# Kernel tuning notes

Measured on AMD Instinct MI355X. Metric: run time of the kernel, lower is better.

Reference implementation:

```python
import jax, jax.numpy as jnp
import numpy as np

B, NN, DEG = 64, 256, 8
N = B * NN
E = N * DEG
IN_N, IN_E = 128, 16
TOOL, PROC = 16, 12
TP = TOOL * PROC
H1 = 384

def _lin(key, i, o, s=0.05):
    k1, k2 = jax.random.split(key)
    return (jax.random.normal(k1, (i, o), jnp.float32) * s,
            jax.random.normal(k2, (o,), jnp.float32) * s)

def setup_inputs():
    ks = jax.random.split(jax.random.key(0), 40)
    inp = {}
    inp["ns"] = jax.random.normal(ks[0], (N, IN_N), jnp.float32)
    inp["es"] = jax.random.normal(ks[1], (E, IN_E), jnp.float32)
    inp["dm"] = jax.random.normal(ks[2], (N, NN), jnp.float32)
    inp["mask_fv"] = (jax.random.uniform(ks[3], (N, TP)) > 0.3).astype(jnp.float32)
    dst = jnp.repeat(jnp.arange(N, dtype=jnp.int32), DEG)  # fixed in-degree DEG
    src = (dst // NN) * NN + jax.random.randint(ks[4], (E,), 0, NN, dtype=jnp.int32)
    inp["src"], inp["dst"] = src, dst
    sizes = [(IN_N, H1), (H1 + 32, H1), (H1, TP)]
    for i, (cin, cout) in enumerate(sizes, 1):
        inp[f"Wm{i}"], inp[f"bm{i}"] = _lin(ks[5 + 3 * i], 2 * cin + IN_E, cin)
        inp[f"Wu{i}"], inp[f"bu{i}"] = _lin(ks[6 + 3 * i], 5 * cin, cout)
        inp[f"bng{i}"] = jnp.ones((cout,), jnp.float32)
        inp[f"bnb{i}"] = jnp.zeros((cout,), jnp.float32)
        inp[f"Wx{i}"], inp[f"bx{i}"] = _lin(ks[7 + 3 * i], cout, cout)
    inp["W1"], inp["b1"] = _lin(ks[20], NN, 64)
    inp["W2"], inp["b2"] = _lin(ks[21], 64, 32)
    inp["W3"], inp["b3"] = _lin(ks[22], NN, 64)
    inp["W4"], inp["b4"] = _lin(ks[23], 64, NN)
    return inp

def pna_conv(src, dst, h, e, Wm, bm, Wu, bu, bng, bnb, Wx, bx, relu_out):
    # DGL PNAConvTower: msg = M(cat(h_src, h_dst, e)); aggregate mean/max/sum/std per dst node;
    # U(cat(h, aggs)); BatchNorm (training stats); mixing Linear + LeakyReLU(0.01).
    cin = h.shape[1]
    msg = h[src] @ Wm[:cin] + h[dst] @ Wm[cin:2 * cin] + e @ Wm[2 * cin:] + bm  # [E, cin]
    cnt = jax.ops.segment_sum(jnp.ones((msg.shape[0],), msg.dtype), dst, N)[:, None]
    s = jax.ops.segment_sum(msg, dst, N)
    mean = s / cnt
    mx = jax.ops.segment_max(msg, dst, N)
    msq = jax.ops.segment_sum(msg * msg, dst, N) / cnt
    std = jnp.sqrt(jax.nn.relu(msq - mean * mean) + 1e-30)
    u = jnp.concatenate([h, mean, mx, s, std], axis=-1) @ Wu + bu  # [N, cout]
    u = (u - u.mean(0)) / jnp.sqrt(u.var(0) + 1e-5) * bng + bnb  # BatchNorm1d, training mode
    out = jax.nn.leaky_relu(u @ Wx + bx, 0.01)  # mixing layer
    return jax.nn.relu(out) if relu_out else out

def reference(ns, es, dm, mask_fv, Wm1, bm1, Wu1, bu1, bng1, bnb1, Wx1, bx1, Wm2, bm2, Wu2, bu2, bng2, bnb2, Wx2, bx2, Wm3, bm3, Wu3, bu3, bng3, bnb3, Wx3, bx3, W1, b1, W2, b2, W3, b3, W4, b4, src, dst):
    d2 = (dm @ W1 + b1) @ W2 + b2  # [N, 32]
    h1 = pna_conv(src, dst, ns, es, Wm1, bm1, Wu1, bu1, bng1, bnb1, Wx1, bx1, True)
    h2 = pna_conv(src, dst, jnp.concatenate([h1, d2], -1), es, Wm2, bm2, Wu2, bu2, bng2, bnb2, Wx2, bx2, True)
    h3 = pna_conv(src, dst, h2, es, Wm3, bm3, Wu3, bu3, bng3, bnb3, Wx3, bx3, False)  # [N, TP]
    nm = h3.max(-1).reshape(B, NN)
    g = jax.nn.sigmoid(jax.nn.relu(nm @ W3 + b3) @ W4 + b4)  # [B, NN]
    feat = (g.reshape(N, 1) * h3).reshape(B, -1)  # [B, NN*TP]
    feat = jnp.where(mask_fv.reshape(B, -1) == 0, -1e5, feat)
    return jax.nn.softmax(feat, -1)
```

## Files before the change

### kernel.cpp

```cpp
#include <hip/hip_runtime.h>
#include <hip/hip_bf16.h>

#define NNODE 16384

typedef short v8s __attribute__((ext_vector_type(8)));
typedef float v4f __attribute__((ext_vector_type(4)));

__device__ __forceinline__ unsigned short f2bf(float v) {
    unsigned u = __float_as_uint(v);
    unsigned r = (u + 0x7FFF + ((u >> 16) & 1)) >> 16;
    return (unsigned short)r;
}
__device__ __forceinline__ float bf2f(unsigned short s) {
    return __uint_as_float(((unsigned)s) << 16);
}

template<int EPI, int OUT, int BM>
__global__ __launch_bounds__(256, 3)
void mgemm4(const unsigned short* __restrict__ Ah, const unsigned short* __restrict__ Al,
            int ldA, int K,
            const unsigned short* __restrict__ Bh, const unsigned short* __restrict__ Bl,
            int Kpad,
            float* __restrict__ Cf, unsigned short* __restrict__ Ch, unsigned short* __restrict__ Cl,
            int ldC, int Ncol, const float* __restrict__ bias)
{
    constexpr int MF = BM / 32;
    __shared__ __align__(16) unsigned short AhS[BM * 64];
    __shared__ __align__(16) unsigned short AlS[BM * 64];
    __shared__ __align__(16) unsigned short BhS[64 * 64];
    __shared__ __align__(16) unsigned short BlS[64 * 64];
    const int bm = blockIdx.x * BM;
    const int bn = blockIdx.y * 64;
    const int tid = threadIdx.x;
    const int lane = tid & 63, wid = tid >> 6;
    const int wm = wid >> 1, wn = wid & 1;
    const int r16 = lane & 15, q = lane >> 4;
    v4f acc[MF][2];
#pragma unroll
    for (int i = 0; i < MF; i++)
#pragma unroll
        for (int j = 0; j < 2; j++) acc[i][j] = (v4f){0.f, 0.f, 0.f, 0.f};

    const int srow = tid >> 3;
    const int sc8  = tid & 7;
    const int nK = (K + 63) >> 6;
    for (int s = 0; s < nK; s++) {
        const int k0 = s << 6;
#pragma unroll
        for (int p = 0; p < BM / 32; p++) {
            int row = p * 32 + srow;
            size_t go = (size_t)(bm + row) * ldA + k0 + sc8 * 8;
            v8s hv = *(const v8s*)(const void*)(Ah + go);
            v8s lv = *(const v8s*)(const void*)(Al + go);
            int bo = row * 128 + ((sc8 * 16) ^ ((row & 7) << 4));
            *(v8s*)(void*)((char*)AhS + bo) = hv;
            *(v8s*)(void*)((char*)AlS + bo) = lv;
        }
#pragma unroll
        for (int p = 0; p < 2; p++) {
            int row = p * 32 + srow;
            size_t go = (size_t)(bn + row) * Kpad + k0 + sc8 * 8;
            v8s hv = *(const v8s*)(const void*)(Bh + go);
            v8s lv = *(const v8s*)(const void*)(Bl + go);
            int bo = row * 128 + ((sc8 * 16) ^ ((row & 7) << 4));
            *(v8s*)(void*)((char*)BhS + bo) = hv;
            *(v8s*)(void*)((char*)BlS + bo) = lv;
        }
        __syncthreads();
#pragma unroll
        for (int kc = 0; kc < 2; kc++) {
            v8s bh[2], bl[2];
#pragma unroll
            for (int nf = 0; nf < 2; nf++) {
                int bcol = wn * 32 + nf * 16 + r16;
                int bo = bcol * 128 + (((kc * 64) + q * 16) ^ ((bcol & 7) << 4));
                bh[nf] = *(const v8s*)(const void*)((const char*)BhS + bo);
                bl[nf] = *(const v8s*)(const void*)((const char*)BlS + bo);
            }
#pragma unroll
            for (int mf = 0; mf < MF; mf++) {
                int arow = wm * (BM / 2) + mf * 16 + r16;
                int ao = arow * 128 + (((kc * 64) + q * 16) ^ ((arow & 7) << 4));
                v8s ah = *(const v8s*)(const void*)((const char*)AhS + ao);
                v8s al = *(const v8s*)(const void*)((const char*)AlS + ao);
#pragma unroll
                for (int nf = 0; nf < 2; nf++) {
                    acc[mf][nf] = __builtin_amdgcn_mfma_f32_16x16x32_bf16(ah, bh[nf], acc[mf][nf], 0, 0, 0);
                    acc[mf][nf] = __builtin_amdgcn_mfma_f32_16x16x32_bf16(al, bh[nf], acc[mf][nf], 0, 0, 0);
                    acc[mf][nf] = __builtin_amdgcn_mfma_f32_16x16x32_bf16(ah, bl[nf], acc[mf][nf], 0, 0, 0);
                }
            }
        }
        __syncthreads();
    }
#pragma unroll
    for (int mf = 0; mf < MF; mf++)
#pragma unroll
        for (int nf = 0; nf < 2; nf++) {
            int col = bn + wn * 32 + nf * 16 + r16;
            if (col < Ncol) {
                float bv = bias ? bias[col] : 0.f;
#pragma unroll
                for (int r = 0; r < 4; r++) {
                    int row = bm + wm * (BM / 2) + mf * 16 + q * 4 + r;
                    float v = acc[mf][nf][r] + bv;
                    if (EPI == 1) v = fmaxf(v, 0.f);
                    if (EPI == 2) v = (v > 0.f) ? v : 0.01f * v;
                    size_t o = (size_t)row * ldC + col;
                    if (OUT == 0) {
                        Cf[o] = v;
                    } else {
                        unsigned short h = f2bf(v);
                        Ch[o] = h;
                        Cl[o] = f2bf(v - bf2f(h));
                    }
                }
            }
        }
}

__global__ void prep_bt(const float* __restrict__ W, unsigned short* __restrict__ Bh,
                        unsigned short* __restrict__ Bl, int K, int N, int Kpad, int Npad)
{
    int idx = blockIdx.x * 256 + threadIdx.x;
    if (idx >= Npad * Kpad) return;
    int n = idx / Kpad, k = idx % Kpad;
    float v = (n < N && k < K) ? W[(size_t)k * N + n] : 0.f;
    unsigned short h = f2bf(v);
    Bh[idx] = h;
    Bl[idx] = f2bf(v - bf2f(h));
}

__global__ void prep_wu(const float* __restrict__ Wu, unsigned short* __restrict__ Bh,
                        unsigned short* __restrict__ Bl, int cin, int cout, int Npad)
{
    int Kpad = 4 * cin;
    int idx = blockIdx.x * 256 + threadIdx.x;
    if (idx >= Npad * Kpad) return;
    int n = idx / Kpad, k = idx % Kpad;
    float v = 0.f;
    if (n < cout) {
        int qq = k / cin, r = k - qq * cin;
        if (qq == 0)      v = Wu[(size_t)r * cout + n];
        else if (qq == 1) v = Wu[(size_t)(cin + r) * cout + n] * 0.125f + Wu[(size_t)(3 * cin + r) * cout + n];
        else if (qq == 2) v = Wu[(size_t)(2 * cin + r) * cout + n];
        else              v = Wu[(size_t)(4 * cin + r) * cout + n];
    }
    unsigned short h = f2bf(v);
    Bh[idx] = h;
    Bl[idx] = f2bf(v - bf2f(h));
}

__global__ void prep_wx(const float* __restrict__ Wx, const float* __restrict__ scale,
                        unsigned short* __restrict__ Bh, unsigned short* __restrict__ Bl,
                        int K, int N, int Kpad, int Npad)
{
    int idx = blockIdx.x * 256 + threadIdx.x;
    if (idx >= Npad * Kpad) return;
    int n = idx / Kpad, k = idx % Kpad;
    float v = (n < N && k < K) ? Wx[(size_t)k * N + n] * scale[k] : 0.f;
    unsigned short h = f2bf(v);
    Bh[idx] = h;
    Bl[idx] = f2bf(v - bf2f(h));
}

__global__ __launch_bounds__(256) void bias2p_k(const float* __restrict__ Wx,
    const float* __restrict__ bx, const float* __restrict__ shift,
    float* __restrict__ bias2, int K, int N)
{
    int n = blockIdx.x, tid = threadIdx.x;
    float s = 0.f;
    for (int k = tid; k < K; k += 256) s = fmaf(shift[k], Wx[(size_t)k * N + n], s);
    __shared__ float red[256];
    red[tid] = s; __syncthreads();
    for (int st = 128; st > 0; st >>= 1) { if (tid < st) red[tid] += red[tid + st]; __syncthreads(); }
    if (tid == 0) bias2[n] = red[0] + bx[n];
}

__global__ void prep_biasH(const float* __restrict__ bm, float* __restrict__ biasH, int cin)
{
    int i = blockIdx.x * 256 + threadIdx.x;
    if (i < 2 * cin) biasH[i] = (i < cin) ? 0.f : bm[i - cin];
}

__global__ void csplit_k(const float* __restrict__ src, int ldS, int w,
                         unsigned short* __restrict__ Xh, unsigned short* __restrict__ Xl,
                         int ldX, int offX)
{
    int idx = blockIdx.x * 256 + threadIdx.x;
    if (idx >= NNODE * w) return;
    int rrow = idx / w, c = idx - rrow * w;
    float v = src[(size_t)rrow * ldS + c];
    unsigned short h = f2bf(v);
    size_t o = (size_t)rrow * ldX + offX + c;
    Xh[o] = h;
    Xl[o] = f2bf(v - bf2f(h));
}

__global__ __launch_bounds__(256)
void gemm_k(const float* __restrict__ A, const float* __restrict__ Bw,
            float* __restrict__ C, int Ncol, int K, const float* __restrict__ bias)
{
    __shared__ float As[16][128];
    __shared__ float Bs[16][64];
    const int bm = blockIdx.y * 128;
    const int bn = blockIdx.x * 64;
    const int tid = threadIdx.x;
    const int tx = tid & 15, ty = tid >> 4;
    float acc[8][4];
#pragma unroll
    for (int i = 0; i < 8; i++)
#pragma unroll
        for (int j = 0; j < 4; j++) acc[i][j] = 0.f;

    for (int k0 = 0; k0 < K; k0 += 16) {
#pragma unroll
        for (int i = 0; i < 2; i++) {
            int idx = tid * 2 + i;
            int row = idx >> 2;
            int k4  = (idx & 3) << 2;
            const float* ap = A + (size_t)(bm + row) * K + k0 + k4;
            float4 v = *reinterpret_cast<const float4*>(ap);
            As[k4 + 0][row] = v.x;
            As[k4 + 1][row] = v.y;
            As[k4 + 2][row] = v.z;
            As[k4 + 3][row] = v.w;
        }
        {
            int row = tid >> 4;
            int c4  = (tid & 15) << 2;
            int gn  = bn + c4;
            float4 v;
            if (gn + 3 < Ncol) {
                v = *reinterpret_cast<const float4*>(Bw + (size_t)(k0 + row) * Ncol + gn);
            } else {
                float t0 = (gn + 0 < Ncol) ? Bw[(size_t)(k0 + row) * Ncol + gn + 0] : 0.f;
                float t1 = (gn + 1 < Ncol) ? Bw[(size_t)(k0 + row) * Ncol + gn + 1] : 0.f;
                float t2 = (gn + 2 < Ncol) ? Bw[(size_t)(k0 + row) * Ncol + gn + 2] : 0.f;
                float t3 = (gn + 3 < Ncol) ? Bw[(size_t)(k0 + row) * Ncol + gn + 3] : 0.f;
                v = make_float4(t0, t1, t2, t3);
            }
            *reinterpret_cast<float4*>(&Bs[row][c4]) = v;
        }
        __syncthreads();
#pragma unroll
        for (int kk = 0; kk < 16; kk++) {
            float a0[8], b0[4];
#pragma unroll
            for (int i = 0; i < 8; i++) a0[i] = As[kk][ty * 8 + i];
#pragma unroll
            for (int j = 0; j < 4; j++) b0[j] = Bs[kk][tx * 4 + j];
#pragma unroll
            for (int i = 0; i < 8; i++)
#pragma unroll
                for (int j = 0; j < 4; j++) acc[i][j] = fmaf(a0[i], b0[j], acc[i][j]);
        }
        __syncthreads();
    }
#pragma unroll
    for (int i = 0; i < 8; i++) {
        int r = bm + ty * 8 + i;
#pragma unroll
        for (int j = 0; j < 4; j++) {
            int c = bn + tx * 4 + j;
            if (c < Ncol) C[(size_t)r * Ncol + c] = acc[i][j] + (bias ? bias[c] : 0.f);
        }
    }
}

__global__ __launch_bounds__(256)
void agg2_k(const float* __restrict__ H2, const float* __restrict__ es,
            const int* __restrict__ src, const float* __restrict__ Wme,
            unsigned short* __restrict__ Xh, unsigned short* __restrict__ Xl,
            int cin, int ldH, int ldX, int offX)
{
    const int g = blockIdx.x;
    const int c0 = blockIdx.y * 64;
    const int qz = blockIdx.z;
    const int tid = threadIdx.x;
    const int nl = tid >> 6, c = tid & 63;
    const int cc = c0 + c;
    const bool act = cc < cin;
    __shared__ float esl[4][128];
    __shared__ int srcl[512];
    {
        int e0 = g * 2048 + qz * 512;
        for (int i = tid; i < 512; i += 256) srcl[i] = src[e0 + i] - g * 256;
    }
    float wreg[16];
#pragma unroll
    for (int j = 0; j < 16; j++) wreg[j] = act ? Wme[j * cin + cc] : 0.f;
    __syncthreads();
    const float* Hsrc = H2 + (size_t)(g * 256) * ldH + c0;
    const float* Hdst = H2 + (size_t)(g * 256) * ldH + cin + c0;
    for (int i = 0; i < 16; i++) {
        const int vl = qz * 64 + i * 4 + nl;
        {
            const float* ep = es + (size_t)(g * 256 + vl) * 128;
            esl[nl][c] = ep[c];
            esl[nl][64 + c] = ep[64 + c];
        }
        __syncthreads();
        if (act) {
            float hd = Hdst[(size_t)vl * ldH + c];
            float sum = 0.f, sq = 0.f, mx = -INFINITY;
#pragma unroll
            for (int e = 0; e < 8; e++) {
                int sl = srcl[(i * 4 + nl) * 8 + e];
                float m = hd + Hsrc[(size_t)sl * ldH + c];
                float4 e0 = *(const float4*)&esl[nl][e * 16 + 0];
                float4 e1 = *(const float4*)&esl[nl][e * 16 + 4];
                float4 e2 = *(const float4*)&esl[nl][e * 16 + 8];
                float4 e3 = *(const float4*)&esl[nl][e * 16 + 12];
                m = fmaf(e0.x, wreg[0], m);  m = fmaf(e0.y, wreg[1], m);
                m = fmaf(e0.z, wreg[2], m);  m = fmaf(e0.w, wreg[3], m);
                m = fmaf(e1.x, wreg[4], m);  m = fmaf(e1.y, wreg[5], m);
                m = fmaf(e1.z, wreg[6], m);  m = fmaf(e1.w, wreg[7], m);
                m = fmaf(e2.x, wreg[8], m);  m = fmaf(e2.y, wreg[9], m);
                m = fmaf(e2.z, wreg[10], m); m = fmaf(e2.w, wreg[11], m);
                m = fmaf(e3.x, wreg[12], m); m = fmaf(e3.y, wreg[13], m);
                m = fmaf(e3.z, wreg[14], m); m = fmaf(e3.w, wreg[15], m);
                sum += m;
                sq = fmaf(m, m, sq);
                mx = fmaxf(mx, m);
            }
            float mean = sum * 0.125f, msq = sq * 0.125f;
            float stdv = sqrtf(fmaxf(msq - mean * mean, 0.f) + 1e-30f);
            size_t o = (size_t)(g * 256 + vl) * ldX + offX + cc;
            unsigned short h;
            h = f2bf(sum);  Xh[o] = h;            Xl[o] = f2bf(sum - bf2f(h));
            h = f2bf(mx);   Xh[o + cin] = h;      Xl[o + cin] = f2bf(mx - bf2f(h));
            h = f2bf(stdv); Xh[o + 2 * cin] = h;  Xl[o + 2 * cin] = f2bf(stdv - bf2f(h));
        }
        __syncthreads();
    }
}

__global__ void bnstats1s_k(const unsigned short* __restrict__ uh, const unsigned short* __restrict__ ul,
                            float* __restrict__ part, int cout)
{
    int c = threadIdx.x;
    if (c >= cout) return;
    int r0 = blockIdx.x * 256;
    float s = 0.f, q = 0.f;
    for (int r = r0; r < r0 + 256; r++) {
        size_t o = (size_t)r * cout + c;
        float v = bf2f(uh[o]) + bf2f(ul[o]);
        s += v;
        q = fmaf(v, v, q);
    }
    part[(size_t)blockIdx.x * cout + c] = s;
    part[(size_t)(64 + blockIdx.x) * cout + c] = q;
}

__global__ void bnstats2_k(const float* __restrict__ part, const float* __restrict__ bng,
                           const float* __restrict__ bnb, float* __restrict__ scale,
                           float* __restrict__ shift, int cout)
{
    int c = threadIdx.x;
    if (c >= cout) return;
    float s = 0.f, q = 0.f;
    for (int b = 0; b < 64; b++) { s += part[(size_t)b * cout + c]; q += part[(size_t)(64 + b) * cout + c]; }
    float mean = s / 16384.f;
    float var  = q / 16384.f - mean * mean;
    float sc   = bng[c] / sqrtf(var + 1e-5f);
    scale[c] = sc;
    shift[c] = bnb[c] - mean * sc;
}

__global__ void rowmax_k(const float* __restrict__ h3, float* __restrict__ nm)
{
    int wave = threadIdx.x >> 6;
    int lane = threadIdx.x & 63;
    int node = blockIdx.x * 4 + wave;
    const float* row = h3 + (size_t)node * 192;
    float m = -INFINITY;
    for (int t = lane; t < 192; t += 64) m = fmaxf(m, row[t]);
#pragma unroll
    for (int off = 32; off > 0; off >>= 1) m = fmaxf(m, __shfl_down(m, off, 64));
    if (lane == 0) nm[node] = m;
}

__global__ __launch_bounds__(256) void g_k(const float* __restrict__ nm,
    const float* __restrict__ W3, const float* __restrict__ b3,
    const float* __restrict__ W4, const float* __restrict__ b4,
    float* __restrict__ g)
{
    __shared__ float row[256];
    __shared__ float t1[64];
    int b = blockIdx.x, tid = threadIdx.x;
    row[tid] = nm[b * 256 + tid];
    __syncthreads();
    if (tid < 64) {
        float a = b3[tid];
        for (int k = 0; k < 256; k++) a = fmaf(row[k], W3[k * 64 + tid], a);
        t1[tid] = fmaxf(a, 0.f);
    }
    __syncthreads();
    float a = b4[tid];
    for (int j = 0; j < 64; j++) a = fmaf(t1[j], W4[j * 256 + tid], a);
    g[b * 256 + tid] = 1.f / (1.f + expf(-a));
}

__global__ __launch_bounds__(256) void sm1_k(const float* __restrict__ mask,
    const float* __restrict__ g, const float* __restrict__ h3, float* __restrict__ part)
{
    int b = blockIdx.x, s = blockIdx.y, tid = threadIdx.x;
    float l[24];
#pragma unroll
    for (int t = 0; t < 24; t++) {
        int i = s * 6144 + t * 256 + tid;
        size_t idx = (size_t)b * 49152 + i;
        float mk = mask[idx];
        l[t] = (mk == 0.f) ? -1e5f : g[b * 256 + i / 192] * h3[idx];
    }
    float m = -INFINITY;
#pragma unroll
    for (int t = 0; t < 24; t++) m = fmaxf(m, l[t]);
    __shared__ float red[256];
    red[tid] = m; __syncthreads();
    for (int st = 128; st > 0; st >>= 1) { if (tid < st) red[tid] = fmaxf(red[tid], red[tid + st]); __syncthreads(); }
    m = red[0]; __syncthreads();
    float z = 0.f;
#pragma unroll
    for (int t = 0; t < 24; t++) z += expf(l[t] - m);
    red[tid] = z; __syncthreads();
    for (int st = 128; st > 0; st >>= 1) { if (tid < st) red[tid] += red[tid + st]; __syncthreads(); }
    if (tid == 0) { part[(b * 8 + s) * 2] = m; part[(b * 8 + s) * 2 + 1] = red[0]; }
}

__global__ void sm2_k(const float* __restrict__ part, float* __restrict__ mz)
{
    int b = threadIdx.x;
    if (b >= 64) return;
    float M = -INFINITY;
    for (int s = 0; s < 8; s++) M = fmaxf(M, part[(b * 8 + s) * 2]);
    float Z = 0.f;
    for (int s = 0; s < 8; s++) Z += part[(b * 8 + s) * 2 + 1] * expf(part[(b * 8 + s) * 2] - M);
    mz[b * 2] = M;
    mz[b * 2 + 1] = 1.f / Z;
}

__global__ __launch_bounds__(256) void sm3_k(const float* __restrict__ mask,
    const float* __restrict__ g, const float* __restrict__ h3,
    const float* __restrict__ mz, float* __restrict__ out)
{
    int b = blockIdx.x, s = blockIdx.y, tid = threadIdx.x;
    float M = mz[b * 2], invZ = mz[b * 2 + 1];
#pragma unroll
    for (int t = 0; t < 24; t++) {
        int i = s * 6144 + t * 256 + tid;
        size_t idx = (size_t)b * 49152 + i;
        float mk = mask[idx];
        float v = (mk == 0.f) ? -1e5f : g[b * 256 + i / 192] * h3[idx];
        out[idx] = expf(v - M) * invZ;
    }
}

extern "C" void kernel_launch(void* const* d_in, const int* in_sizes, int n_in,
                              void* d_out, int out_size, void* d_ws, size_t ws_size,
                              hipStream_t stream)
{
    const float* ns   = (const float*)d_in[0];
    const float* es   = (const float*)d_in[1];
    const float* dm   = (const float*)d_in[2];
    const float* mask = (const float*)d_in[3];
    const int*   src  = (const int*)d_in[4];
    const float* Wm1 = (const float*)d_in[6],  *bm1 = (const float*)d_in[7];
    const float* Wu1 = (const float*)d_in[8],  *bu1 = (const float*)d_in[9];
    const float* bng1= (const float*)d_in[10], *bnb1= (const float*)d_in[11];
    const float* Wx1 = (const float*)d_in[12], *bx1 = (const float*)d_in[13];
    const float* Wm2 = (const float*)d_in[14], *bm2 = (const float*)d_in[15];
    const float* Wu2 = (const float*)d_in[16], *bu2 = (const float*)d_in[17];
    const float* bng2= (const float*)d_in[18], *bnb2= (const float*)d_in[19];
    const float* Wx2 = (const float*)d_in[20], *bx2 = (const float*)d_in[21];
    const float* Wm3 = (const float*)d_in[22], *bm3 = (const float*)d_in[23];
    const float* Wu3 = (const float*)d_in[24], *bu3 = (const float*)d_in[25];
    const float* bng3= (const float*)d_in[26], *bnb3= (const float*)d_in[27];
    const float* Wx3 = (const float*)d_in[28], *bx3 = (const float*)d_in[29];
    const float* W1 = (const float*)d_in[30], *b1 = (const float*)d_in[31];
    const float* W2 = (const float*)d_in[32], *b2 = (const float*)d_in[33];
    const float* W3 = (const float*)d_in[34], *b3 = (const float*)d_in[35];
    const float* W4 = (const float*)d_in[36], *b4 = (const float*)d_in[37];
    float* out = (float*)d_out;

    const int N = NNODE;
    char* base = (char*)d_ws;
    size_t off = 0;
    auto alloc = [&](size_t bytes) -> void* {
        void* p = base + off;
        off = (off + bytes + 255) & ~(size_t)255;
        return p;
    };
    unsigned short* Xh = (unsigned short*)alloc((size_t)N * 1664 * 2);
    unsigned short* Xl = (unsigned short*)alloc((size_t)N * 1664 * 2);
    float* H2   = (float*)alloc((size_t)N * 832 * 4);
    unsigned short* uh = (unsigned short*)alloc((size_t)N * 384 * 2);
    unsigned short* ul = (unsigned short*)alloc((size_t)N * 384 * 2);
    float* h3b  = (float*)alloc((size_t)N * 192 * 4);
    float* d2f  = (float*)alloc((size_t)N * 32 * 4);
    float* part = (float*)alloc((size_t)128 * 384 * 4);
    float* scale= (float*)alloc(384 * 4);
    float* shift= (float*)alloc(384 * 4);
    float* bias2= (float*)alloc(384 * 4);
    float* biasH1 = (float*)alloc(256 * 4);
    float* biasH2 = (float*)alloc(832 * 4);
    float* biasH3 = (float*)alloc(768 * 4);
    float* nm   = (float*)alloc((size_t)N * 4);
    float* gbuf = (float*)alloc((size_t)N * 4);
    float* smp  = (float*)alloc(64 * 8 * 2 * 4);
    float* smz  = (float*)alloc(64 * 2 * 4);
    auto aw = [&](size_t elems) -> unsigned short* { return (unsigned short*)alloc(elems * 2); };
    unsigned short *BWm1h = aw(256 * 128),   *BWm1l = aw(256 * 128);
    unsigned short *BWu1h = aw(384 * 512),   *BWu1l = aw(384 * 512);
    unsigned short *BWx1h = aw(384 * 384),   *BWx1l = aw(384 * 384);
    unsigned short *BWm2h = aw(896 * 448),   *BWm2l = aw(896 * 448);
    unsigned short *BWu2h = aw(384 * 1664),  *BWu2l = aw(384 * 1664);
    unsigned short *BWx2h = aw(384 * 384),   *BWx2l = aw(384 * 384);
    unsigned short *BWm3h = aw(768 * 384),   *BWm3l = aw(768 * 384);
    unsigned short *BWu3h = aw(256 * 1536),  *BWu3l = aw(256 * 1536);
    unsigned short *BWx3h = aw(256 * 192),   *BWx3l = aw(256 * 192);

    auto gp = [](size_t n) { return dim3((unsigned)((n + 255) / 256)); };

    prep_bt<<<gp(128 * 128), 256, 0, stream>>>(Wm1,             BWm1h,             BWm1l,             128, 128, 128, 128);
    prep_bt<<<gp(128 * 128), 256, 0, stream>>>(Wm1 + 128 * 128, BWm1h + 128 * 128, BWm1l + 128 * 128, 128, 128, 128, 128);
    prep_wu<<<gp(384 * 512), 256, 0, stream>>>(Wu1, BWu1h, BWu1l, 128, 384, 384);
    prep_bt<<<gp(416 * 448), 256, 0, stream>>>(Wm2,             BWm2h,             BWm2l,             416, 416, 448, 416);
    prep_bt<<<gp(480 * 448), 256, 0, stream>>>(Wm2 + 416 * 416, BWm2h + 416 * 448, BWm2l + 416 * 448, 416, 416, 448, 480);
    prep_wu<<<gp(384 * 1664), 256, 0, stream>>>(Wu2, BWu2h, BWu2l, 416, 384, 384);
    prep_bt<<<gp(384 * 384), 256, 0, stream>>>(Wm3,             BWm3h,             BWm3l,             384, 384, 384, 384);
    prep_bt<<<gp(384 * 384), 256, 0, stream>>>(Wm3 + 384 * 384, BWm3h + 384 * 384, BWm3l + 384 * 384, 384, 384, 384, 384);
    prep_wu<<<gp(256 * 1536), 256, 0, stream>>>(Wu3, BWu3h, BWu3l, 384, 192, 256);
    prep_biasH<<<gp(256), 256, 0, stream>>>(bm1, biasH1, 128);
    prep_biasH<<<gp(832), 256, 0, stream>>>(bm2, biasH2, 416);
    prep_biasH<<<gp(768), 256, 0, stream>>>(bm3, biasH3, 384);

    csplit_k<<<gp((size_t)N * 128), 256, 0, stream>>>(ns, 128, 128, Xh, Xl, 512, 0);

    gemm_k<<<dim3(1, 128), 256, 0, stream>>>(dm, W1, H2, 64, 256, b1);
    gemm_k<<<dim3(1, 128), 256, 0, stream>>>(H2, W2, d2f, 32, 64, b2);

    mgemm4<0, 0, 128><<<dim3(128, 4), 256, 0, stream>>>(Xh, Xl, 512, 128, BWm1h, BWm1l, 128,
                                                        H2, nullptr, nullptr, 256, 256, biasH1);
    agg2_k<<<dim3(64, 2, 4), 256, 0, stream>>>(H2, es, src, Wm1 + 2 * 128 * 128, Xh, Xl, 128, 256, 512, 128);
    mgemm4<0, 1, 128><<<dim3(128, 6), 256, 0, stream>>>(Xh, Xl, 512, 512, BWu1h, BWu1l, 512,
                                                        nullptr, uh, ul, 384, 384, bu1);
    bnstats1s_k<<<64, 384, 0, stream>>>(uh, ul, part, 384);
    bnstats2_k<<<1, 384, 0, stream>>>(part, bng1, bnb1, scale, shift, 384);
    prep_wx<<<gp(384 * 384), 256, 0, stream>>>(Wx1, scale, BWx1h, BWx1l, 384, 384, 384, 384);
    bias2p_k<<<384, 256, 0, stream>>>(Wx1, bx1, shift, bias2, 384, 384);
    mgemm4<1, 1, 128><<<dim3(128, 6), 256, 0, stream>>>(uh, ul, 384, 384, BWx1h, BWx1l, 384,
                                                        nullptr, Xh, Xl, 1664, 384, bias2);
    csplit_k<<<gp((size_t)N * 32), 256, 0, stream>>>(d2f, 32, 32, Xh, Xl, 1664, 384);

    mgemm4<0, 0, 128><<<dim3(128, 13), 256, 0, stream>>>(Xh, Xl, 1664, 416, BWm2h, BWm2l, 448,
                                                         H2, nullptr, nullptr, 832, 832, biasH2);
    agg2_k<<<dim3(64, 7, 4), 256, 0, stream>>>(H2, es, src, Wm2 + 2 * 416 * 416, Xh, Xl, 416, 832, 1664, 416);
    mgemm4<0, 1, 128><<<dim3(128, 6), 256, 0, stream>>>(Xh, Xl, 1664, 1664, BWu2h, BWu2l, 1664,
                                                        nullptr, uh, ul, 384, 384, bu2);
    bnstats1s_k<<<64, 384, 0, stream>>>(uh, ul, part, 384);
    bnstats2_k<<<1, 384, 0, stream>>>(part, bng2, bnb2, scale, shift, 384);
    prep_wx<<<gp(384 * 384), 256, 0, stream>>>(Wx2, scale, BWx2h, BWx2l, 384, 384, 384, 384);
    bias2p_k<<<384, 256, 0, stream>>>(Wx2, bx2, shift, bias2, 384, 384);
    mgemm4<1, 1, 128><<<dim3(128, 6), 256, 0, stream>>>(uh, ul, 384, 384, BWx2h, BWx2l, 384,
                                                        nullptr, Xh, Xl, 1536, 384, bias2);

    mgemm4<0, 0, 128><<<dim3(128, 12), 256, 0, stream>>>(Xh, Xl, 1536, 384, BWm3h, BWm3l, 384,
                                                         H2, nullptr, nullptr, 768, 768, biasH3);
    agg2_k<<<dim3(64, 6, 4), 256, 0, stream>>>(H2, es, src, Wm3 + 2 * 384 * 384, Xh, Xl, 384, 768, 1536, 384);
    mgemm4<0, 1, 64><<<dim3(256, 3), 256, 0, stream>>>(Xh, Xl, 1536, 1536, BWu3h, BWu3l, 1536,
                                                       nullptr, uh, ul, 192, 192, bu3);
    bnstats1s_k<<<64, 384, 0, stream>>>(uh, ul, part, 192);
    bnstats2_k<<<1, 384, 0, stream>>>(part, bng3, bnb3, scale, shift, 192);
    prep_wx<<<gp(256 * 192), 256, 0, stream>>>(Wx3, scale, BWx3h, BWx3l, 192, 192, 192, 256);
    bias2p_k<<<192, 256, 0, stream>>>(Wx3, bx3, shift, bias2, 192, 192);
    mgemm4<2, 0, 64><<<dim3(256, 3), 256, 0, stream>>>(uh, ul, 192, 192, BWx3h, BWx3l, 192,
                                                       h3b, nullptr, nullptr, 192, 192, bias2);

    rowmax_k<<<N / 4, 256, 0, stream>>>(h3b, nm);
    g_k<<<64, 256, 0, stream>>>(nm, W3, b3, W4, b4, gbuf);
    sm1_k<<<dim3(64, 8), 256, 0, stream>>>(mask, gbuf, h3b, smp);
    sm2_k<<<1, 64, 0, stream>>>(smp, smz);
    sm3_k<<<dim3(64, 8), 256, 0, stream>>>(mask, gbuf, h3b, smz, out);
}
```

Before: 678.3 us.

## Pre-swizzle weights into MFMA fragment layout and fold h-term of update GEMM into message GEMM

Weights are repacked into a per-lane MFMA fragment layout, so the GEMM kernel loads B operands straight from global memory into registers instead of staging them through LDS. This frees LDS and allows raising occupancy to 4 blocks per CU. The h-part of the update projection (Wu rows for h) is appended as extra output columns of the message GEMM. The update GEMM then only covers the aggregate features, with K cut from 4*cin to 3*cin, and adds the precomputed h contribution in its epilogue. The trade-offs are redundant per-wave B loads from global or L2 in place of shared LDS reuse, plus an extra fp32 read in the epilogue.

```diff
diff --git a/kernel.cpp b/kernel.cpp
--- a/kernel.cpp
+++ b/kernel.cpp
@@ -5,30 +5,29 @@
 
 typedef short v8s __attribute__((ext_vector_type(8)));
 typedef float v4f __attribute__((ext_vector_type(4)));
-
-__device__ __forceinline__ unsigned short f2bf(float v) {
+typedef unsigned short us16;
+
+__device__ __forceinline__ us16 f2bf(float v) {
     unsigned u = __float_as_uint(v);
     unsigned r = (u + 0x7FFF + ((u >> 16) & 1)) >> 16;
-    return (unsigned short)r;
-}
-__device__ __forceinline__ float bf2f(unsigned short s) {
+    return (us16)r;
+}
+__device__ __forceinline__ float bf2f(us16 s) {
     return __uint_as_float(((unsigned)s) << 16);
 }
 
-template<int EPI, int OUT, int BM>
-__global__ __launch_bounds__(256, 3)
-void mgemm4(const unsigned short* __restrict__ Ah, const unsigned short* __restrict__ Al,
+template<int EPI, int OUT, int ACC, int BM>
+__global__ __launch_bounds__(256, 4)
+void mgemm5(const us16* __restrict__ Ah, const us16* __restrict__ Al,
             int ldA, int K,
-            const unsigned short* __restrict__ Bh, const unsigned short* __restrict__ Bl,
-            int Kpad,
-            float* __restrict__ Cf, unsigned short* __restrict__ Ch, unsigned short* __restrict__ Cl,
+            const us16* __restrict__ Bh, const us16* __restrict__ Bl, int KC,
+            const float* __restrict__ CfIn, int ldCin,
+            float* __restrict__ Cf, us16* __restrict__ Ch, us16* __restrict__ Cl,
             int ldC, int Ncol, const float* __restrict__ bias)
 {
     constexpr int MF = BM / 32;
-    __shared__ __align__(16) unsigned short AhS[BM * 64];
-    __shared__ __align__(16) unsigned short AlS[BM * 64];
-    __shared__ __align__(16) unsigned short BhS[64 * 64];
-    __shared__ __align__(16) unsigned short BlS[64 * 64];
+    __shared__ __align__(16) us16 AhS[BM * 64];
+    __shared__ __align__(16) us16 AlS[BM * 64];
     const int bm = blockIdx.x * BM;
     const int bn = blockIdx.y * 64;
     const int tid = threadIdx.x;
@@ -43,6 +42,7 @@
 
     const int srow = tid >> 3;
     const int sc8  = tid & 7;
+    const int cb0  = (bn >> 4) + wn * 2;
     const int nK = (K + 63) >> 6;
     for (int s = 0; s < nK; s++) {
         const int k0 = s << 6;
@@ -56,27 +56,20 @@
             *(v8s*)(void*)((char*)AhS + bo) = hv;
             *(v8s*)(void*)((char*)AlS + bo) = lv;
         }
-#pragma unroll
-        for (int p = 0; p < 2; p++) {
-            int row = p * 32 + srow;
-            size_t go = (size_t)(bn + row) * Kpad + k0 + sc8 * 8;
-            v8s hv = *(const v8s*)(const void*)(Bh + go);
-            v8s lv = *(const v8s*)(const void*)(Bl + go);
-            int bo = row * 128 + ((sc8 * 16) ^ ((row & 7) << 4));
-            *(v8s*)(void*)((char*)BhS + bo) = hv;
-            *(v8s*)(void*)((char*)BlS + bo) = lv;
+        v8s Bfh[2][2], Bfl[2][2];
+#pragma unroll
+        for (int kc = 0; kc < 2; kc++) {
+            int kchunk = (k0 >> 5) + kc;
+#pragma unroll
+            for (int nf = 0; nf < 2; nf++) {
+                size_t fo = ((size_t)((cb0 + nf) * KC + kchunk) * 64 + lane) * 8;
+                Bfh[kc][nf] = *(const v8s*)(const void*)(Bh + fo);
+                Bfl[kc][nf] = *(const v8s*)(const void*)(Bl + fo);
+            }
         }
         __syncthreads();
 #pragma unroll
         for (int kc = 0; kc < 2; kc++) {
-            v8s bh[2], bl[2];
-#pragma unroll
-            for (int nf = 0; nf < 2; nf++) {
-                int bcol = wn * 32 + nf * 16 + r16;
-                int bo = bcol * 128 + (((kc * 64) + q * 16) ^ ((bcol & 7) << 4));
-                bh[nf] = *(const v8s*)(const void*)((const char*)BhS + bo);
-                bl[nf] = *(const v8s*)(const void*)((const char*)BlS + bo);
-            }
 #pragma unroll
             for (int mf = 0; mf < MF; mf++) {
                 int arow = wm * (BM / 2) + mf * 16 + r16;
@@ -85,9 +78,9 @@
                 v8s al = *(const v8s*)(const void*)((const char*)AlS + ao);
 #pragma unroll
                 for (int nf = 0; nf < 2; nf++) {
-                    acc[mf][nf] = __builtin_amdgcn_mfma_f32_16x16x32_bf16(ah, bh[nf], acc[mf][nf], 0, 0, 0);
-                    acc[mf][nf] = __builtin_amdgcn_mfma_f32_16x16x32_bf16(al, bh[nf], acc[mf][nf], 0, 0, 0);
-                    acc[mf][nf] = __builtin_amdgcn_mfma_f32_16x16x32_bf16(ah, bl[nf], acc[mf][nf], 0, 0, 0);
+                    acc[mf][nf] = __builtin_amdgcn_mfma_f32_16x16x32_bf16(ah, Bfh[kc][nf], acc[mf][nf], 0, 0, 0);
+                    acc[mf][nf] = __builtin_amdgcn_mfma_f32_16x16x32_bf16(al, Bfh[kc][nf], acc[mf][nf], 0, 0, 0);
+                    acc[mf][nf] = __builtin_amdgcn_mfma_f32_16x16x32_bf16(ah, Bfl[kc][nf], acc[mf][nf], 0, 0, 0);
                 }
             }
         }
@@ -104,13 +97,14 @@
                 for (int r = 0; r < 4; r++) {
                     int row = bm + wm * (BM / 2) + mf * 16 + q * 4 + r;
                     float v = acc[mf][nf][r] + bv;
+                    if (ACC) v += CfIn[(size_t)row * ldCin + col];
                     if (EPI == 1) v = fmaxf(v, 0.f);
                     if (EPI == 2) v = (v > 0.f) ? v : 0.01f * v;
                     size_t o = (size_t)row * ldC + col;
                     if (OUT == 0) {
                         Cf[o] = v;
                     } else {
-                        unsigned short h = f2bf(v);
+                        us16 h = f2bf(v);
                         Ch[o] = h;
                         Cl[o] = f2bf(v - bf2f(h));
                     }
@@ -119,47 +113,55 @@
         }
 }
 
-__global__ void prep_bt(const float* __restrict__ W, unsigned short* __restrict__ Bh,
-                        unsigned short* __restrict__ Bl, int K, int N, int Kpad, int Npad)
+__global__ void prep_fr_bt(const float* __restrict__ W, int ldW,
+                           us16* __restrict__ Bh, us16* __restrict__ Bl,
+                           int K, int N, int KC)
 {
     int idx = blockIdx.x * 256 + threadIdx.x;
-    if (idx >= Npad * Kpad) return;
-    int n = idx / Kpad, k = idx % Kpad;
-    float v = (n < N && k < K) ? W[(size_t)k * N + n] : 0.f;
-    unsigned short h = f2bf(v);
+    if (idx >= N * KC * 32) return;
+    int e = idx & 7, lane = (idx >> 3) & 63, rem = idx >> 9;
+    int kchunk = rem % KC, colblk = rem / KC;
+    int n = colblk * 16 + (lane & 15);
+    int k = kchunk * 32 + (lane >> 4) * 8 + e;
+    float v = (k < K && n < N) ? W[(size_t)k * ldW + n] : 0.f;
+    us16 h = f2bf(v);
     Bh[idx] = h;
     Bl[idx] = f2bf(v - bf2f(h));
 }
 
-__global__ void prep_wu(const float* __restrict__ Wu, unsigned short* __restrict__ Bh,
-                        unsigned short* __restrict__ Bl, int cin, int cout, int Npad)
-{
-    int Kpad = 4 * cin;
+__global__ void prep_fr_wu(const float* __restrict__ Wu,
+                           us16* __restrict__ Bh, us16* __restrict__ Bl,
+                           int cin, int cout, int KC)
+{
     int idx = blockIdx.x * 256 + threadIdx.x;
-    if (idx >= Npad * Kpad) return;
-    int n = idx / Kpad, k = idx % Kpad;
+    if (idx >= cout * KC * 32) return;
+    int e = idx & 7, lane = (idx >> 3) & 63, rem = idx >> 9;
+    int kchunk = rem % KC, colblk = rem / KC;
+    int n = colblk * 16 + (lane & 15);
+    int k = kchunk * 32 + (lane >> 4) * 8 + e;
     float v = 0.f;
-    if (n < cout) {
-        int qq = k / cin, r = k - qq * cin;
-        if (qq == 0)      v = Wu[(size_t)r * cout + n];
-        else if (qq == 1) v = Wu[(size_t)(cin + r) * cout + n] * 0.125f + Wu[(size_t)(3 * cin + r) * cout + n];
-        else if (qq == 2) v = Wu[(size_t)(2 * cin + r) * cout + n];
-        else              v = Wu[(size_t)(4 * cin + r) * cout + n];
-    }
-    unsigned short h = f2bf(v);
+    if (n < cout && k < 3 * cin) {
+        if (k < cin)          v = Wu[(size_t)(cin + k) * cout + n] * 0.125f + Wu[(size_t)(3 * cin + k) * cout + n];
+        else if (k < 2 * cin) v = Wu[(size_t)(2 * cin + (k - cin)) * cout + n];
+        else                  v = Wu[(size_t)(4 * cin + (k - 2 * cin)) * cout + n];
+    }
+    us16 h = f2bf(v);
     Bh[idx] = h;
     Bl[idx] = f2bf(v - bf2f(h));
 }
 
-__global__ void prep_wx(const float* __restrict__ Wx, const float* __restrict__ scale,
-                        unsigned short* __restrict__ Bh, unsigned short* __restrict__ Bl,
-                        int K, int N, int Kpad, int Npad)
+__global__ void prep_fr_wx(const float* __restrict__ Wx, const float* __restrict__ scale,
+                           us16* __restrict__ Bh, us16* __restrict__ Bl,
+                           int K, int N, int KC)
 {
     int idx = blockIdx.x * 256 + threadIdx.x;
-    if (idx >= Npad * Kpad) return;
-    int n = idx / Kpad, k = idx % Kpad;
-    float v = (n < N && k < K) ? Wx[(size_t)k * N + n] * scale[k] : 0.f;
-    unsigned short h = f2bf(v);
+    if (idx >= N * KC * 32) return;
+    int e = idx & 7, lane = (idx >> 3) & 63, rem = idx >> 9;
+    int kchunk = rem % KC, colblk = rem / KC;
+    int n = colblk * 16 + (lane & 15);
+    int k = kchunk * 32 + (lane >> 4) * 8 + e;
+    float v = (k < K && n < N) ? Wx[(size_t)k * N + n] * scale[k] : 0.f;
+    us16 h = f2bf(v);
     Bh[idx] = h;
     Bl[idx] = f2bf(v - bf2f(h));
 }
@@ -177,21 +179,27 @@
     if (tid == 0) bias2[n] = red[0] + bx[n];
 }
 
-__global__ void prep_biasH(const float* __restrict__ bm, float* __restrict__ biasH, int cin)
+__global__ void prep_biasMU(const float* __restrict__ bm, const float* __restrict__ bu,
+                            float* __restrict__ o, int cin, int cout)
 {
     int i = blockIdx.x * 256 + threadIdx.x;
-    if (i < 2 * cin) biasH[i] = (i < cin) ? 0.f : bm[i - cin];
+    if (i >= 2 * cin + cout) return;
+    float v;
+    if (i < cin)          v = 0.f;
+    else if (i < 2 * cin) v = bm[i - cin];
+    else                  v = bu[i - 2 * cin];
+    o[i] = v;
 }
 
 __global__ void csplit_k(const float* __restrict__ src, int ldS, int w,
-                         unsigned short* __restrict__ Xh, unsigned short* __restrict__ Xl,
+                         us16* __restrict__ Xh, us16* __restrict__ Xl,
                          int ldX, int offX)
 {
     int idx = blockIdx.x * 256 + threadIdx.x;
     if (idx >= NNODE * w) return;
     int rrow = idx / w, c = idx - rrow * w;
     float v = src[(size_t)rrow * ldS + c];
-    unsigned short h = f2bf(v);
+    us16 h = f2bf(v);
     size_t o = (size_t)rrow * ldX + offX + c;
     Xh[o] = h;
     Xl[o] = f2bf(v - bf2f(h));
@@ -271,7 +279,7 @@
 __global__ __launch_bounds__(256)
 void agg2_k(const float* __restrict__ H2, const float* __restrict__ es,
             const int* __restrict__ src, const float* __restrict__ Wme,
-            unsigned short* __restrict__ Xh, unsigned short* __restrict__ Xl,
+            us16* __restrict__ Xh, us16* __restrict__ Xl,
             int cin, int ldH, int ldX, int offX)
 {
     const int g = blockIdx.x;
@@ -327,7 +335,7 @@
             float mean = sum * 0.125f, msq = sq * 0.125f;
             float stdv = sqrtf(fmaxf(msq - mean * mean, 0.f) + 1e-30f);
             size_t o = (size_t)(g * 256 + vl) * ldX + offX + cc;
-            unsigned short h;
+            us16 h;
             h = f2bf(sum);  Xh[o] = h;            Xl[o] = f2bf(sum - bf2f(h));
             h = f2bf(mx);   Xh[o + cin] = h;      Xl[o + cin] = f2bf(mx - bf2f(h));
             h = f2bf(stdv); Xh[o + 2 * cin] = h;  Xl[o + 2 * cin] = f2bf(stdv - bf2f(h));
@@ -336,7 +344,7 @@
     }
 }
 
-__global__ void bnstats1s_k(const unsigned short* __restrict__ uh, const unsigned short* __restrict__ ul,
+__global__ void bnstats1s_k(const us16* __restrict__ uh, const us16* __restrict__ ul,
                             float* __restrict__ part, int cout)
 {
     int c = threadIdx.x;
@@ -492,91 +500,95 @@
         off = (off + bytes + 255) & ~(size_t)255;
         return p;
     };
-    unsigned short* Xh = (unsigned short*)alloc((size_t)N * 1664 * 2);
-    unsigned short* Xl = (unsigned short*)alloc((size_t)N * 1664 * 2);
-    float* H2   = (float*)alloc((size_t)N * 832 * 4);
-    unsigned short* uh = (unsigned short*)alloc((size_t)N * 384 * 2);
-    unsigned short* ul = (unsigned short*)alloc((size_t)N * 384 * 2);
+    us16* Xh = (us16*)alloc((size_t)N * 1728 * 2);
+    us16* Xl = (us16*)alloc((size_t)N * 1728 * 2);
+    float* H2   = (float*)alloc((size_t)N * 1216 * 4);
+    us16* uh = (us16*)alloc((size_t)N * 384 * 2);
+    us16* ul = (us16*)alloc((size_t)N * 384 * 2);
     float* h3b  = (float*)alloc((size_t)N * 192 * 4);
     float* d2f  = (float*)alloc((size_t)N * 32 * 4);
     float* part = (float*)alloc((size_t)128 * 384 * 4);
     float* scale= (float*)alloc(384 * 4);
     float* shift= (float*)alloc(384 * 4);
     float* bias2= (float*)alloc(384 * 4);
-    float* biasH1 = (float*)alloc(256 * 4);
-    float* biasH2 = (float*)alloc(832 * 4);
-    float* biasH3 = (float*)alloc(768 * 4);
+    float* biasMU1 = (float*)alloc(640 * 4);
+    float* biasMU2 = (float*)alloc(1216 * 4);
+    float* biasMU3 = (float*)alloc(960 * 4);
     float* nm   = (float*)alloc((size_t)N * 4);
     float* gbuf = (float*)alloc((size_t)N * 4);
     float* smp  = (float*)alloc(64 * 8 * 2 * 4);
     float* smz  = (float*)alloc(64 * 2 * 4);
-    auto aw = [&](size_t elems) -> unsigned short* { return (unsigned short*)alloc(elems * 2); };
-    unsigned short *BWm1h = aw(256 * 128),   *BWm1l = aw(256 * 128);
-    unsigned short *BWu1h = aw(384 * 512),   *BWu1l = aw(384 * 512);
-    unsigned short *BWx1h = aw(384 * 384),   *BWx1l = aw(384 * 384);
-    unsigned short *BWm2h = aw(896 * 448),   *BWm2l = aw(896 * 448);
-    unsigned short *BWu2h = aw(384 * 1664),  *BWu2l = aw(384 * 1664);
-    unsigned short *BWx2h = aw(384 * 384),   *BWx2l = aw(384 * 384);
-    unsigned short *BWm3h = aw(768 * 384),   *BWm3l = aw(768 * 384);
-    unsigned short *BWu3h = aw(256 * 1536),  *BWu3l = aw(256 * 1536);
-    unsigned short *BWx3h = aw(256 * 192),   *BWx3l = aw(256 * 192);
+    auto aw = [&](size_t elems) -> us16* { return (us16*)alloc(elems * 2); };
+    us16 *BM1h = aw((size_t)640 * 128),   *BM1l = aw((size_t)640 * 128);
+    us16 *BA1h = aw((size_t)384 * 384),   *BA1l = aw((size_t)384 * 384);
+    us16 *BX1h = aw((size_t)384 * 384),   *BX1l = aw((size_t)384 * 384);
+    us16 *BM2h = aw((size_t)1216 * 448),  *BM2l = aw((size_t)1216 * 448);
+    us16 *BA2h = aw((size_t)384 * 1280),  *BA2l = aw((size_t)384 * 1280);
+    us16 *BX2h = aw((size_t)384 * 384),   *BX2l = aw((size_t)384 * 384);
+    us16 *BM3h = aw((size_t)960 * 384),   *BM3l = aw((size_t)960 * 384);
+    us16 *BA3h = aw((size_t)192 * 1152),  *BA3l = aw((size_t)192 * 1152);
+    us16 *BX3h = aw((size_t)192 * 192),   *BX3l = aw((size_t)192 * 192);
 
     auto gp = [](size_t n) { return dim3((unsigned)((n + 255) / 256)); };
-
-    prep_bt<<<gp(128 * 128), 256, 0, stream>>>(Wm1,             BWm1h,             BWm1l,             128, 128, 128, 128);
-    prep_bt<<<gp(128 * 128), 256, 0, stream>>>(Wm1 + 128 * 128, BWm1h + 128 * 128, BWm1l + 128 * 128, 128, 128, 128, 128);
-    prep_wu<<<gp(384 * 512), 256, 0, stream>>>(Wu1, BWu1h, BWu1l, 128, 384, 384);
-    prep_bt<<<gp(416 * 448), 256, 0, stream>>>(Wm2,             BWm2h,             BWm2l,             416, 416, 448, 416);
-    prep_bt<<<gp(480 * 448), 256, 0, stream>>>(Wm2 + 416 * 416, BWm2h + 416 * 448, BWm2l + 416 * 448, 416, 416, 448, 480);
-    prep_wu<<<gp(384 * 1664), 256, 0, stream>>>(Wu2, BWu2h, BWu2l, 416, 384, 384);
-    prep_bt<<<gp(384 * 384), 256, 0, stream>>>(Wm3,             BWm3h,             BWm3l,             384, 384, 384, 384);
-    prep_bt<<<gp(384 * 384), 256, 0, stream>>>(Wm3 + 384 * 384, BWm3h + 384 * 384, BWm3l + 384 * 384, 384, 384, 384, 384);
-    prep_wu<<<gp(256 * 1536), 256, 0, stream>>>(Wu3, BWu3h, BWu3l, 384, 192, 256);
-    prep_biasH<<<gp(256), 256, 0, stream>>>(bm1, biasH1, 128);
-    prep_biasH<<<gp(832), 256, 0, stream>>>(bm2, biasH2, 416);
-    prep_biasH<<<gp(768), 256, 0, stream>>>(bm3, biasH3, 384);
+    auto fsec = [](us16* b, int c0, int KC) { return b + (size_t)(c0 / 16) * KC * 512; };
+
+    prep_fr_bt<<<gp((size_t)128 * 128), 256, 0, stream>>>(Wm1,             128, fsec(BM1h, 0, 4),   fsec(BM1l, 0, 4),   128, 128, 4);
+    prep_fr_bt<<<gp((size_t)128 * 128), 256, 0, stream>>>(Wm1 + 128 * 128, 128, fsec(BM1h, 128, 4), fsec(BM1l, 128, 4), 128, 128, 4);
+    prep_fr_bt<<<gp((size_t)384 * 128), 256, 0, stream>>>(Wu1,             384, fsec(BM1h, 256, 4), fsec(BM1l, 256, 4), 128, 384, 4);
+    prep_fr_wu<<<gp((size_t)384 * 384), 256, 0, stream>>>(Wu1, BA1h, BA1l, 128, 384, 12);
+    prep_fr_bt<<<gp((size_t)416 * 448), 256, 0, stream>>>(Wm2,             416, fsec(BM2h, 0, 14),   fsec(BM2l, 0, 14),   416, 416, 14);
+    prep_fr_bt<<<gp((size_t)416 * 448), 256, 0, stream>>>(Wm2 + 416 * 416, 416, fsec(BM2h, 416, 14), fsec(BM2l, 416, 14), 416, 416, 14);
+    prep_fr_bt<<<gp((size_t)384 * 448), 256, 0, stream>>>(Wu2,             384, fsec(BM2h, 832, 14), fsec(BM2l, 832, 14), 416, 384, 14);
+    prep_fr_wu<<<gp((size_t)384 * 1280), 256, 0, stream>>>(Wu2, BA2h, BA2l, 416, 384, 40);
+    prep_fr_bt<<<gp((size_t)384 * 384), 256, 0, stream>>>(Wm3,             384, fsec(BM3h, 0, 12),   fsec(BM3l, 0, 12),   384, 384, 12);
+    prep_fr_bt<<<gp((size_t)384 * 384), 256, 0, stream>>>(Wm3 + 384 * 384, 384, fsec(BM3h, 384, 12), fsec(BM3l, 384, 12), 384, 384, 12);
+    prep_fr_bt<<<gp((size_t)192 * 384), 256, 0, stream>>>(Wu3,             192, fsec(BM3h, 768, 12), fsec(BM3l, 768, 12), 384, 192, 12);
+    prep_fr_wu<<<gp((size_t)192 * 1152), 256, 0, stream>>>(Wu3, BA3h, BA3l, 384, 192, 36);
+    prep_biasMU<<<gp(640), 256, 0, stream>>>(bm1, bu1, biasMU1, 128, 384);
+    prep_biasMU<<<gp(1216), 256, 0, stream>>>(bm2, bu2, biasMU2, 416, 384);
+    prep_biasMU<<<gp(960), 256, 0, stream>>>(bm3, bu3, biasMU3, 384, 192);
 
     csplit_k<<<gp((size_t)N * 128), 256, 0, stream>>>(ns, 128, 128, Xh, Xl, 512, 0);
 
     gemm_k<<<dim3(1, 128), 256, 0, stream>>>(dm, W1, H2, 64, 256, b1);
     gemm_k<<<dim3(1, 128), 256, 0, stream>>>(H2, W2, d2f, 32, 64, b2);
 
-    mgemm4<0, 0, 128><<<dim3(128, 4), 256, 0, stream>>>(Xh, Xl, 512, 128, BWm1h, BWm1l, 128,
-                                                        H2, nullptr, nullptr, 256, 256, biasH1);
-    agg2_k<<<dim3(64, 2, 4), 256, 0, stream>>>(H2, es, src, Wm1 + 2 * 128 * 128, Xh, Xl, 128, 256, 512, 128);
-    mgemm4<0, 1, 128><<<dim3(128, 6), 256, 0, stream>>>(Xh, Xl, 512, 512, BWu1h, BWu1l, 512,
-                                                        nullptr, uh, ul, 384, 384, bu1);
+    mgemm5<0, 0, 0, 128><<<dim3(128, 10), 256, 0, stream>>>(Xh, Xl, 512, 128, BM1h, BM1l, 4,
+        nullptr, 0, H2, nullptr, nullptr, 640, 640, biasMU1);
+    agg2_k<<<dim3(64, 2, 4), 256, 0, stream>>>(H2, es, src, Wm1 + 2 * 128 * 128, Xh, Xl, 128, 640, 512, 128);
+    mgemm5<0, 1, 1, 128><<<dim3(128, 6), 256, 0, stream>>>(Xh + 128, Xl + 128, 512, 384, BA1h, BA1l, 12,
+        H2 + 256, 640, nullptr, uh, ul, 384, 384, nullptr);
     bnstats1s_k<<<64, 384, 0, stream>>>(uh, ul, part, 384);
     bnstats2_k<<<1, 384, 0, stream>>>(part, bng1, bnb1, scale, shift, 384);
-    prep_wx<<<gp(384 * 384), 256, 0, stream>>>(Wx1, scale, BWx1h, BWx1l, 384, 384, 384, 384);
+    prep_fr_wx<<<gp((size_t)384 * 384), 256, 0, stream>>>(Wx1, scale, BX1h, BX1l, 384, 384, 12);
     bias2p_k<<<384, 256, 0, stream>>>(Wx1, bx1, shift, bias2, 384, 384);
-    mgemm4<1, 1, 128><<<dim3(128, 6), 256, 0, stream>>>(uh, ul, 384, 384, BWx1h, BWx1l, 384,
-                                                        nullptr, Xh, Xl, 1664, 384, bias2);
-    csplit_k<<<gp((size_t)N * 32), 256, 0, stream>>>(d2f, 32, 32, Xh, Xl, 1664, 384);
-
-    mgemm4<0, 0, 128><<<dim3(128, 13), 256, 0, stream>>>(Xh, Xl, 1664, 416, BWm2h, BWm2l, 448,
-                                                         H2, nullptr, nullptr, 832, 832, biasH2);
-    agg2_k<<<dim3(64, 7, 4), 256, 0, stream>>>(H2, es, src, Wm2 + 2 * 416 * 416, Xh, Xl, 416, 832, 1664, 416);
-    mgemm4<0, 1, 128><<<dim3(128, 6), 256, 0, stream>>>(Xh, Xl, 1664, 1664, BWu2h, BWu2l, 1664,
-                                                        nullptr, uh, ul, 384, 384, bu2);
+    mgemm5<1, 1, 0, 128><<<dim3(128, 6), 256, 0, stream>>>(uh, ul, 384, 384, BX1h, BX1l, 12,
+        nullptr, 0, nullptr, Xh, Xl, 1728, 384, bias2);
+    csplit_k<<<gp((size_t)N * 32), 256, 0, stream>>>(d2f, 32, 32, Xh, Xl, 1728, 384);
+
+    mgemm5<0, 0, 0, 128><<<dim3(128, 19), 256, 0, stream>>>(Xh, Xl, 1728, 416, BM2h, BM2l, 14,
+        nullptr, 0, H2, nullptr, nullptr, 1216, 1216, biasMU2);
+    agg2_k<<<dim3(64, 7, 4), 256, 0, stream>>>(H2, es, src, Wm2 + 2 * 416 * 416, Xh, Xl, 416, 1216, 1728, 416);
+    mgemm5<0, 1, 1, 128><<<dim3(128, 6), 256, 0, stream>>>(Xh + 416, Xl + 416, 1728, 1248, BA2h, BA2l, 40,
+        H2 + 832, 1216, nullptr, uh, ul, 384, 384, nullptr);
     bnstats1s_k<<<64, 384, 0, stream>>>(uh, ul, part, 384);
     bnstats2_k<<<1, 384, 0, stream>>>(part, bng2, bnb2, scale, shift, 384);
-    prep_wx<<<gp(384 * 384), 256, 0, stream>>>(Wx2, scale, BWx2h, BWx2l, 384, 384, 384, 384);
+    prep_fr_wx<<<gp((size_t)384 * 384), 256, 0, stream>>>(Wx2, scale, BX2h, BX2l, 384, 384, 12);
     bias2p_k<<<384, 256, 0, stream>>>(Wx2, bx2, shift, bias2, 384, 384);
-    mgemm4<1, 1, 128><<<dim3(128, 6), 256, 0, stream>>>(uh, ul, 384, 384, BWx2h, BWx2l, 384,
-                                                        nullptr, Xh, Xl, 1536, 384, bias2);
-
-    mgemm4<0, 0, 128><<<dim3(128, 12), 256, 0, stream>>>(Xh, Xl, 1536, 384, BWm3h, BWm3l, 384,
-                                                         H2, nullptr, nullptr, 768, 768, biasH3);
-    agg2_k<<<dim3(64, 6, 4), 256, 0, stream>>>(H2, es, src, Wm3 + 2 * 384 * 384, Xh, Xl, 384, 768, 1536, 384);
-    mgemm4<0, 1, 64><<<dim3(256, 3), 256, 0, stream>>>(Xh, Xl, 1536, 1536, BWu3h, BWu3l, 1536,
-                                                       nullptr, uh, ul, 192, 192, bu3);
+    mgemm5<1, 1, 0, 128><<<dim3(128, 6), 256, 0, stream>>>(uh, ul, 384, 384, BX2h, BX2l, 12,
+        nullptr, 0, nullptr, Xh, Xl, 1536, 384, bias2);
+
+    mgemm5<0, 0, 0, 128><<<dim3(128, 15), 256, 0, stream>>>(Xh, Xl, 1536, 384, BM3h, BM3l, 12,
+        nullptr, 0, H2, nullptr, nullptr, 960, 960, biasMU3);
+    agg2_k<<<dim3(64, 6, 4), 256, 0, stream>>>(H2, es, src, Wm3 + 2 * 384 * 384, Xh, Xl, 384, 960, 1536, 384);
+    mgemm5<0, 1, 1, 64><<<dim3(256, 3), 256, 0, stream>>>(Xh + 384, Xl + 384, 1536, 1152, BA3h, BA3l, 36,
+        H2 + 768, 960, nullptr, uh, ul, 192, 192, nullptr);
     bnstats1s_k<<<64, 384, 0, stream>>>(uh, ul, part, 192);
     bnstats2_k<<<1, 384, 0, stream>>>(part, bng3, bnb3, scale, shift, 192);
-    prep_wx<<<gp(256 * 192), 256, 0, stream>>>(Wx3, scale, BWx3h, BWx3l, 192, 192, 192, 256);
+    prep_fr_wx<<<gp((size_t)192 * 192), 256, 0, stream>>>(Wx3, scale, BX3h, BX3l, 192, 192, 6);
     bias2p_k<<<192, 256, 0, stream>>>(Wx3, bx3, shift, bias2, 192, 192);
-    mgemm4<2, 0, 64><<<dim3(256, 3), 256, 0, stream>>>(uh, ul, 192, 192, BWx3h, BWx3l, 192,
-                                                       h3b, nullptr, nullptr, 192, 192, bias2);
+    mgemm5<2, 0, 0, 64><<<dim3(256, 3), 256, 0, stream>>>(uh, ul, 192, 192, BX3h, BX3l, 6,
+        nullptr, 0, h3b, nullptr, nullptr, 192, 192, bias2);
 
     rowmax_k<<<N / 4, 256, 0, stream>>>(h3b, nm);
     g_k<<<64, 256, 0, stream>>>(nm, W3, b3, W4, b4, gbuf);
```

After: 700.5 us. 3.3% more time.
